# Optimization experiments

Measured on AMD Instinct MI355X. Metric: run time of the kernel, lower is better.

The kernel has to match this reference:

```python
import jax, jax.numpy as jnp
import numpy as np

N, H, W = 2000, 128, 128

def setup_inputs() -> dict:
    key = jax.random.key(0)
    k1, k2, k3, k4 = jax.random.split(key, 4)
    means3D = jax.random.normal(k1, (N, 3), dtype=jnp.float32) * 2.0
    means3D = means3D.at[:, 2].add(10.0)  # put gaussians in front of camera, depth ~in (1,50)
    A = jax.random.normal(k2, (N, 3, 3), dtype=jnp.float32) * 0.1
    covs3d = jnp.einsum('nij,nkj->nik', A, A) + 1e-3 * jnp.eye(3, dtype=jnp.float32)
    colors = jax.random.uniform(k3, (N, 3), dtype=jnp.float32)
    opacities = jax.random.uniform(k4, (N,), dtype=jnp.float32)
    fx = fy = 100.0
    K = jnp.array([[fx, 0.0, W / 2.0], [0.0, fy, H / 2.0], [0.0, 0.0, 1.0]], dtype=jnp.float32)
    R = jnp.eye(3, dtype=jnp.float32)
    t = jnp.zeros((3,), dtype=jnp.float32)
    y, x = jnp.meshgrid(jnp.arange(H, dtype=jnp.float32), jnp.arange(W, dtype=jnp.float32), indexing='ij')
    pixels = jnp.stack([x, y], axis=-1)  # (H, W, 2)
    return {"means3D": means3D, "covs3d": covs3d, "colors": colors,
            "opacities": opacities, "K": K, "R": R, "t": t, "pixels": pixels}

def _render(means3D, covs3d, colors, opacities, K, R, t, pixels):
    # --- projection ---
    cam = means3D @ R.T + t                       # (N,3)
    depths = jnp.clip(cam[:, 2], 1.0, None)       # clamp(min=1.0)
    screen = cam @ K.T
    means2D = screen[:, :2] / screen[:, 2:3]      # (N,2)
    fx, fy = K[0, 0], K[1, 1]
    tx, ty, tz = cam[:, 0], cam[:, 1], cam[:, 2]
    z = jnp.zeros_like(tz)
    J = jnp.stack([jnp.stack([fx / tz, z, -fx * tx / (tz * tz)], -1),
                   jnp.stack([z, fy / tz, -fy * ty / (tz * tz)], -1)], -2)  # (N,2,3)
    covs_cam = jnp.einsum('ij,njk,lk->nil', R, covs3d, R)                   # R C R^T
    covs2D = jnp.einsum('nij,njk,nlk->nil', J, covs_cam, J)                 # (N,2,2)
    valid = (depths > 1.0) & (depths < 50.0)
    # --- depth sort (front to back) ---
    idx = jnp.argsort(depths)
    means2D = means2D[idx]; covs2D = covs2D[idx]
    colors = colors[idx]; opacities = opacities[idx]; valid = valid[idx]
    # --- per-pixel gaussian values ---
    covs2D = covs2D + 1e-4 * jnp.eye(2, dtype=covs2D.dtype)
    a, b = covs2D[:, 0, 0], covs2D[:, 0, 1]
    c, d = covs2D[:, 1, 0], covs2D[:, 1, 1]
    det = a * d - b * c                            # (N,)
    inv = jnp.stack([jnp.stack([d, -b], -1), jnp.stack([-c, a], -1)], -2) / det[:, None, None]
    dx = pixels[None] - means2D[:, None, None, :]  # (N,H,W,2)
    expnum = -jnp.einsum('nhwi,nij,nhwj->nhw', dx, inv, dx)
    gauss = jnp.exp(expnum) / (2.0 * jnp.pi * jnp.sqrt(det))[:, None, None]  # (N,H,W)
    gauss = gauss * valid[:, None, None].astype(gauss.dtype)
    # --- alpha compositing ---
    alphas = opacities[:, None, None] * gauss                   # (N,H,W)
    cum = jnp.cumprod(1.0 - alphas, axis=0)
    trans = jnp.concatenate([jnp.ones((1,) + alphas.shape[1:], alphas.dtype), cum[1:]], axis=0)
    weights = alphas * trans                                    # (N,H,W)
    rendered = jnp.einsum('nhw,nc->hwc', weights, colors)       # (H,W,3)
    return rendered

def reference(means3D, covs3d, colors, opacities, K, R, t, pixels):
    return _render(means3D, covs3d, colors, opacities, K, R, t, pixels)
```

## Files before the change

kernel.cpp:

```cpp
#include <hip/hip_runtime.h>
#include <math.h>

#define NGAUSS 2000
#define IMW 128
#define IMH 128
#define NPIX (IMW*IMH)
#define PSTRIDE 12
#define NW 16
#define SEGSZ ((NGAUSS + NW - 1) / NW)

__device__ inline float rdlane(float x, int l) {
    return __uint_as_float(__builtin_amdgcn_readlane(__float_as_uint(x), l));
}

__global__ __launch_bounds__(64) void preprank_kernel(
    const float* __restrict__ means3D, const float* __restrict__ covs3d,
    const float* __restrict__ colors, const float* __restrict__ opac,
    const float* __restrict__ Km, const float* __restrict__ Rm,
    const float* __restrict__ tv, float* __restrict__ sorted)
{
    int i = blockIdx.x;
    int lane = threadIdx.x;

    float R0 = Rm[0], R1 = Rm[1], R2 = Rm[2];
    float R3 = Rm[3], R4 = Rm[4], R5 = Rm[5];
    float R6 = Rm[6], R7 = Rm[7], R8 = Rm[8];
    float t0 = tv[0], t1v = tv[1], t2 = tv[2];

    float mx = means3D[3*i+0], my = means3D[3*i+1], mz = means3D[3*i+2];
    float di = fmaxf(R6*mx + R7*my + R8*mz + t2, 1.0f);
    int rank = 0;
    for (int j = lane; j < NGAUSS; j += 64) {
        float jx = means3D[3*j+0], jy = means3D[3*j+1], jz = means3D[3*j+2];
        float dj = fmaxf(R6*jx + R7*jy + R8*jz + t2, 1.0f);
        bool lt = (j != i) && ((dj < di) || (dj == di && j < i));
        rank += lt ? 1 : 0;
    }
    #pragma unroll
    for (int o = 32; o > 0; o >>= 1) rank += __shfl_down(rank, o, 64);
    rank = __shfl(rank, 0, 64);

    float camx = R0*mx + R1*my + R2*mz + t0;
    float camy = R3*mx + R4*my + R5*mz + t1v;
    float camz = R6*mx + R7*my + R8*mz + t2;
    float depth = fmaxf(camz, 1.0f);
    bool valid = (depth > 1.0f) && (depth < 50.0f);

    float fx = Km[0], cx = Km[2], fy = Km[4], cy = Km[5];
    float invz = 1.0f / camz;
    float m2x = (fx*camx + cx*camz) * invz;
    float m2y = (fy*camy + cy*camz) * invz;
    float J00 = fx*invz, J02 = -fx*camx*invz*invz;
    float J11 = fy*invz, J12 = -fy*camy*invz*invz;

    float S0 = covs3d[9*i+0], S1 = covs3d[9*i+1], S2 = covs3d[9*i+2];
    float S3 = covs3d[9*i+3], S4 = covs3d[9*i+4], S5 = covs3d[9*i+5];
    float S6 = covs3d[9*i+6], S7 = covs3d[9*i+7], S8 = covs3d[9*i+8];

    float RS0 = R0*S0 + R1*S3 + R2*S6;
    float RS1 = R0*S1 + R1*S4 + R2*S7;
    float RS2 = R0*S2 + R1*S5 + R2*S8;
    float RS3 = R3*S0 + R4*S3 + R5*S6;
    float RS4 = R3*S1 + R4*S4 + R5*S7;
    float RS5 = R3*S2 + R4*S5 + R5*S8;
    float RS6 = R6*S0 + R7*S3 + R8*S6;
    float RS7 = R6*S1 + R7*S4 + R8*S7;
    float RS8 = R6*S2 + R7*S5 + R8*S8;

    float Sc0 = RS0*R0 + RS1*R1 + RS2*R2;
    float Sc1 = RS0*R3 + RS1*R4 + RS2*R5;
    float Sc2 = RS0*R6 + RS1*R7 + RS2*R8;
    float Sc3 = RS3*R0 + RS4*R1 + RS5*R2;
    float Sc4 = RS3*R3 + RS4*R4 + RS5*R5;
    float Sc5 = RS3*R6 + RS4*R7 + RS5*R8;
    float Sc6 = RS6*R0 + RS7*R1 + RS8*R2;
    float Sc7 = RS6*R3 + RS7*R4 + RS8*R5;
    float Sc8 = RS6*R6 + RS7*R7 + RS8*R8;

    float A00 = J00*Sc0 + J02*Sc6;
    float A01 = J00*Sc1 + J02*Sc7;
    float A02 = J00*Sc2 + J02*Sc8;
    float A10 = J11*Sc3 + J12*Sc6;
    float A11 = J11*Sc4 + J12*Sc7;
    float A12 = J11*Sc5 + J12*Sc8;

    float a = A00*J00 + A02*J02 + 1e-4f;
    float b = A01*J11 + A02*J12;
    float c = A10*J00 + A12*J02;
    float d = A11*J11 + A12*J12 + 1e-4f;

    float det = a*d - b*c;
    float invdet = 1.0f / det;
    float q0u = d*invdet;
    float q1u = -(b + c)*invdet;
    float q2u = a*invdet;
    float mh = 0.5f*(q0u + q2u);
    float dh = 0.5f*(q0u - q2u);
    float oh = 0.5f*q1u;
    float lmin = mh - sqrtf(dh*dh + oh*oh);
    const float L2E = 1.4426950408889634f;
    float s_cull = lmin * L2E;
    float q0 = -q0u * L2E;
    float q1 = -q1u * L2E;
    float q2 = -q2u * L2E;
    float c0 = opac[i] * 0.15915494309189535f / sqrtf(det);
    if (!valid) { m2x = 0.f; m2y = 0.f; q0 = 0.f; q1 = 0.f; q2 = 0.f; c0 = 0.f; s_cull = 3.0e38f; }

    float cr = colors[3*i+0], cg = colors[3*i+1], cb = colors[3*i+2];
    if (lane < 3) {
        float4 v = (lane == 0) ? make_float4(m2x, m2y, s_cull, q0)
                 : (lane == 1) ? make_float4(q1, q2, c0, cr)
                               : make_float4(cg, cb, depth, 0.f);
        ((float4*)(sorted + (size_t)rank*PSTRIDE))[lane] = v;
    }
}

__global__ __launch_bounds__(1024) void render_fused(
    const float* __restrict__ sorted, float* __restrict__ out)
{
    extern __shared__ char ldsbuf[];
    float*  mxA  = (float*)ldsbuf;
    float*  myA  = mxA + 2048;
    float*  sA   = myA + 2048;
    float*  q0A  = sA + 2048;
    float4* sp2  = (float4*)(q0A + 2048);
    float4* pOut = sp2 + 2*NGAUSS;

    int tid  = threadIdx.x;
    int lane = tid & 63;
    int w    = tid >> 6;
    int bid  = blockIdx.x;
    int row  = bid >> 1;
    int xoff = (bid & 1) * 64;

    for (int g = tid; g < NGAUSS; g += 1024) {
        const float4* src = (const float4*)(sorted + (size_t)g*PSTRIDE);
        float4 v0 = src[0], v1 = src[1], v2 = src[2];
        mxA[g] = v0.x; myA[g] = v0.y; sA[g] = v0.z; q0A[g] = v0.w;
        sp2[g*2] = v1; sp2[g*2+1] = v2;
    }
    __syncthreads();

    float px = (float)(xoff + lane);
    float py = (float)row;
    float x0 = (float)xoff, x1 = x0 + 63.0f;

    float Cr = 0.f, Cg = 0.f, Cb = 0.f, T = 1.f;

    int segBase = w * SEGSZ;
    int segEnd  = segBase + SEGSZ; if (segEnd > NGAUSS) segEnd = NGAUSS;

    for (int cb = segBase; cb < segEnd; cb += 64) {
        int g = cb + lane;
        float cmx = 0.f, cmy = 0.f, cq0 = 0.f;
        bool keep = false;
        if (g < segEnd) {
            cmx = mxA[g]; cmy = myA[g]; cq0 = q0A[g];
            float cs = sA[g];
            float dxm = fmaxf(0.f, fmaxf(x0 - cmx, cmx - x1));
            float dym = fabsf(py - cmy);
            keep = cs * fmaf(dxm, dxm, dym*dym) <= 24.f;
        }
        float4 v1 = make_float4(0.f,0.f,0.f,0.f), v2 = v1;
        if (keep) { v1 = sp2[g*2]; v2 = sp2[g*2+1]; }
        unsigned long long mask = __ballot(keep);
        while (mask) {
            int b = __builtin_ctzll(mask);
            mask &= mask - 1;
            int gn = cb + b;
            float gmx = rdlane(cmx, b), gmy = rdlane(cmy, b), gq0 = rdlane(cq0, b);
            float gq1 = rdlane(v1.x, b), gq2 = rdlane(v1.y, b), gc0 = rdlane(v1.z, b);
            float gcr = rdlane(v1.w, b), gcg = rdlane(v2.x, b), gcb = rdlane(v2.y, b);
            float dy = py - gmy;
            float u2 = fmaf(gq1, dy, 0.f);
            float dx = px - gmx;
            float e  = fmaf(fmaf(gq0, dx, u2), dx, (gq2*dy)*dy);
            float al = gc0 * exp2f(e);
            float wgt = T * al;
            float sel = (gn == 0) ? 0.f : al;
            float f = fmaf(-sel, wgt, wgt);
            Cr = fmaf(f, gcr, Cr);
            Cg = fmaf(f, gcg, Cg);
            Cb = fmaf(f, gcb, Cb);
            T -= wgt;
        }
    }

    pOut[w*64 + lane] = make_float4(Cr, Cg, Cb, T);
    __syncthreads();

    if (tid < 64) {
        float cR = 0.f, cG = 0.f, cB = 0.f, tA = 1.f;
        #pragma unroll
        for (int s = 0; s < NW; ++s) {
            float4 v = pOut[s*64 + tid];
            cR = fmaf(tA, v.x, cR);
            cG = fmaf(tA, v.y, cG);
            cB = fmaf(tA, v.z, cB);
            tA *= v.w;
        }
        int p = row*IMW + xoff + tid;
        out[3*p+0] = cR; out[3*p+1] = cG; out[3*p+2] = cB;
    }
}

extern "C" void kernel_launch(void* const* d_in, const int* in_sizes, int n_in,
                              void* d_out, int out_size, void* d_ws, size_t ws_size,
                              hipStream_t stream)
{
    const float* means3D = (const float*)d_in[0];
    const float* covs3d  = (const float*)d_in[1];
    const float* colors  = (const float*)d_in[2];
    const float* opac    = (const float*)d_in[3];
    const float* Km      = (const float*)d_in[4];
    const float* Rm      = (const float*)d_in[5];
    const float* tv      = (const float*)d_in[6];

    float* sorted = (float*)d_ws;

    preprank_kernel<<<NGAUSS, 64, 0, stream>>>(
        means3D, covs3d, colors, opac, Km, Rm, tv, sorted);

    size_t ldsBytes = 4*2048*sizeof(float)
                    + (size_t)2*NGAUSS*sizeof(float4)
                    + (size_t)NW*64*sizeof(float4);
    render_fused<<<NPIX/64, 1024, ldsBytes, stream>>>(sorted, (float*)d_out);
}
```

Before: 26.97 us.

## Switch sorted gaussian buffer to SoA and load segments directly into registers

The preprocess kernel now writes ten per-gaussian attributes in structure-of-arrays layout and computes rank with ballot+popcount instead of a shuffle reduction. The render kernel drops the block-wide LDS staging of all 2000 gaussians and the barrier that follows it. Each wave instead loads its 125-gaussian segment straight from global memory into registers as two 64-lane chunks. This removes a large LDS fill per block and shrinks shared memory use, but relies on the hardcoded SEGSZ of at most 128 and repeats global loads across blocks, which should mostly hit cache.

Result: faster. 25.77 us (-4.4%).

```diff
diff --git a/kernel.cpp b/kernel.cpp
--- a/kernel.cpp
+++ b/kernel.cpp
@@ -5,7 +5,6 @@
 #define IMW 128
 #define IMH 128
 #define NPIX (IMW*IMH)
-#define PSTRIDE 12
 #define NW 16
 #define SEGSZ ((NGAUSS + NW - 1) / NW)
 
@@ -17,7 +16,7 @@
     const float* __restrict__ means3D, const float* __restrict__ covs3d,
     const float* __restrict__ colors, const float* __restrict__ opac,
     const float* __restrict__ Km, const float* __restrict__ Rm,
-    const float* __restrict__ tv, float* __restrict__ sorted)
+    const float* __restrict__ tv, float* __restrict__ soa)
 {
     int i = blockIdx.x;
     int lane = threadIdx.x;
@@ -30,15 +29,15 @@
     float mx = means3D[3*i+0], my = means3D[3*i+1], mz = means3D[3*i+2];
     float di = fmaxf(R6*mx + R7*my + R8*mz + t2, 1.0f);
     int rank = 0;
-    for (int j = lane; j < NGAUSS; j += 64) {
-        float jx = means3D[3*j+0], jy = means3D[3*j+1], jz = means3D[3*j+2];
+    for (int base = 0; base < 2048; base += 64) {
+        int j = base + lane;
+        int jc = (j < NGAUSS) ? j : 0;
+        float jx = means3D[3*jc+0], jy = means3D[3*jc+1], jz = means3D[3*jc+2];
         float dj = fmaxf(R6*jx + R7*jy + R8*jz + t2, 1.0f);
-        bool lt = (j != i) && ((dj < di) || (dj == di && j < i));
-        rank += lt ? 1 : 0;
-    }
-    #pragma unroll
-    for (int o = 32; o > 0; o >>= 1) rank += __shfl_down(rank, o, 64);
-    rank = __shfl(rank, 0, 64);
+        bool lt = (j < NGAUSS) && (j != i) &&
+                  ((dj < di) || (dj == di && j < i));
+        rank += (int)__popcll(__ballot(lt));
+    }
 
     float camx = R0*mx + R1*my + R2*mz + t0;
     float camy = R3*mx + R4*my + R5*mz + t1v;
@@ -107,24 +106,23 @@
     if (!valid) { m2x = 0.f; m2y = 0.f; q0 = 0.f; q1 = 0.f; q2 = 0.f; c0 = 0.f; s_cull = 3.0e38f; }
 
     float cr = colors[3*i+0], cg = colors[3*i+1], cb = colors[3*i+2];
-    if (lane < 3) {
-        float4 v = (lane == 0) ? make_float4(m2x, m2y, s_cull, q0)
-                 : (lane == 1) ? make_float4(q1, q2, c0, cr)
-                               : make_float4(cg, cb, depth, 0.f);
-        ((float4*)(sorted + (size_t)rank*PSTRIDE))[lane] = v;
-    }
+    float v = (lane == 0) ? m2x
+            : (lane == 1) ? m2y
+            : (lane == 2) ? s_cull
+            : (lane == 3) ? q0
+            : (lane == 4) ? q1
+            : (lane == 5) ? q2
+            : (lane == 6) ? c0
+            : (lane == 7) ? cr
+            : (lane == 8) ? cg
+                          : cb;
+    if (lane < 10) soa[lane*NGAUSS + rank] = v;
 }
 
 __global__ __launch_bounds__(1024) void render_fused(
-    const float* __restrict__ sorted, float* __restrict__ out)
+    const float* __restrict__ soa, float* __restrict__ out)
 {
-    extern __shared__ char ldsbuf[];
-    float*  mxA  = (float*)ldsbuf;
-    float*  myA  = mxA + 2048;
-    float*  sA   = myA + 2048;
-    float*  q0A  = sA + 2048;
-    float4* sp2  = (float4*)(q0A + 2048);
-    float4* pOut = sp2 + 2*NGAUSS;
+    __shared__ float4 pOut[NW*64];
 
     int tid  = threadIdx.x;
     int lane = tid & 63;
@@ -133,14 +131,6 @@
     int row  = bid >> 1;
     int xoff = (bid & 1) * 64;
 
-    for (int g = tid; g < NGAUSS; g += 1024) {
-        const float4* src = (const float4*)(sorted + (size_t)g*PSTRIDE);
-        float4 v0 = src[0], v1 = src[1], v2 = src[2];
-        mxA[g] = v0.x; myA[g] = v0.y; sA[g] = v0.z; q0A[g] = v0.w;
-        sp2[g*2] = v1; sp2[g*2+1] = v2;
-    }
-    __syncthreads();
-
     float px = (float)(xoff + lane);
     float py = (float)row;
     float x0 = (float)xoff, x1 = x0 + 63.0f;
@@ -148,37 +138,63 @@
     float Cr = 0.f, Cg = 0.f, Cb = 0.f, T = 1.f;
 
     int segBase = w * SEGSZ;
-    int segEnd  = segBase + SEGSZ; if (segEnd > NGAUSS) segEnd = NGAUSS;
-
-    for (int cb = segBase; cb < segEnd; cb += 64) {
-        int g = cb + lane;
-        float cmx = 0.f, cmy = 0.f, cq0 = 0.f;
-        bool keep = false;
-        if (g < segEnd) {
-            cmx = mxA[g]; cmy = myA[g]; cq0 = q0A[g];
-            float cs = sA[g];
-            float dxm = fmaxf(0.f, fmaxf(x0 - cmx, cmx - x1));
-            float dym = fabsf(py - cmy);
-            keep = cs * fmaf(dxm, dxm, dym*dym) <= 24.f;
-        }
-        float4 v1 = make_float4(0.f,0.f,0.f,0.f), v2 = v1;
-        if (keep) { v1 = sp2[g*2]; v2 = sp2[g*2+1]; }
+
+    int gA = segBase + lane;
+    bool vB = (64 + lane) < SEGSZ;
+    int gB = vB ? (segBase + 64 + lane) : segBase;
+    float A0 = soa[0*NGAUSS+gA], A1 = soa[1*NGAUSS+gA], A2 = soa[2*NGAUSS+gA];
+    float A3 = soa[3*NGAUSS+gA], A4 = soa[4*NGAUSS+gA], A5 = soa[5*NGAUSS+gA];
+    float A6 = soa[6*NGAUSS+gA], A7 = soa[7*NGAUSS+gA], A8 = soa[8*NGAUSS+gA];
+    float A9 = soa[9*NGAUSS+gA];
+    float B0 = soa[0*NGAUSS+gB], B1 = soa[1*NGAUSS+gB], B2 = soa[2*NGAUSS+gB];
+    float B3 = soa[3*NGAUSS+gB], B4 = soa[4*NGAUSS+gB], B5 = soa[5*NGAUSS+gB];
+    float B6 = soa[6*NGAUSS+gB], B7 = soa[7*NGAUSS+gB], B8 = soa[8*NGAUSS+gB];
+    float B9 = soa[9*NGAUSS+gB];
+
+    {
+        float dxm = fmaxf(0.f, fmaxf(x0 - A0, A0 - x1));
+        float dym = fabsf(py - A1);
+        bool keep = A2 * fmaf(dxm, dxm, dym*dym) <= 24.f;
         unsigned long long mask = __ballot(keep);
         while (mask) {
             int b = __builtin_ctzll(mask);
             mask &= mask - 1;
-            int gn = cb + b;
-            float gmx = rdlane(cmx, b), gmy = rdlane(cmy, b), gq0 = rdlane(cq0, b);
-            float gq1 = rdlane(v1.x, b), gq2 = rdlane(v1.y, b), gc0 = rdlane(v1.z, b);
-            float gcr = rdlane(v1.w, b), gcg = rdlane(v2.x, b), gcb = rdlane(v2.y, b);
+            int gn = segBase + b;
+            float gmx = rdlane(A0,b), gmy = rdlane(A1,b);
+            float gq0 = rdlane(A3,b), gq1 = rdlane(A4,b), gq2 = rdlane(A5,b);
+            float gc0 = rdlane(A6,b), gcr = rdlane(A7,b);
+            float gcg = rdlane(A8,b), gcb = rdlane(A9,b);
             float dy = py - gmy;
-            float u2 = fmaf(gq1, dy, 0.f);
             float dx = px - gmx;
-            float e  = fmaf(fmaf(gq0, dx, u2), dx, (gq2*dy)*dy);
+            float e  = fmaf(fmaf(gq0, dx, gq1*dy), dx, (gq2*dy)*dy);
             float al = gc0 * exp2f(e);
             float wgt = T * al;
             float sel = (gn == 0) ? 0.f : al;
             float f = fmaf(-sel, wgt, wgt);
+            Cr = fmaf(f, gcr, Cr);
+            Cg = fmaf(f, gcg, Cg);
+            Cb = fmaf(f, gcb, Cb);
+            T -= wgt;
+        }
+    }
+    {
+        float dxm = fmaxf(0.f, fmaxf(x0 - B0, B0 - x1));
+        float dym = fabsf(py - B1);
+        bool keep = vB && (B2 * fmaf(dxm, dxm, dym*dym) <= 24.f);
+        unsigned long long mask = __ballot(keep);
+        while (mask) {
+            int b = __builtin_ctzll(mask);
+            mask &= mask - 1;
+            float gmx = rdlane(B0,b), gmy = rdlane(B1,b);
+            float gq0 = rdlane(B3,b), gq1 = rdlane(B4,b), gq2 = rdlane(B5,b);
+            float gc0 = rdlane(B6,b), gcr = rdlane(B7,b);
+            float gcg = rdlane(B8,b), gcb = rdlane(B9,b);
+            float dy = py - gmy;
+            float dx = px - gmx;
+            float e  = fmaf(fmaf(gq0, dx, gq1*dy), dx, (gq2*dy)*dy);
+            float al = gc0 * exp2f(e);
+            float wgt = T * al;
+            float f = fmaf(-al, wgt, wgt);
             Cr = fmaf(f, gcr, Cr);
             Cg = fmaf(f, gcg, Cg);
             Cb = fmaf(f, gcb, Cb);
@@ -216,13 +232,9 @@
     const float* Rm      = (const float*)d_in[5];
     const float* tv      = (const float*)d_in[6];
 
-    float* sorted = (float*)d_ws;
+    float* soa = (float*)d_ws;
 
     preprank_kernel<<<NGAUSS, 64, 0, stream>>>(
-        means3D, covs3d, colors, opac, Km, Rm, tv, sorted);
-
-    size_t ldsBytes = 4*2048*sizeof(float)
-                    + (size_t)2*NGAUSS*sizeof(float4)
-                    + (size_t)NW*64*sizeof(float4);
-    render_fused<<<NPIX/64, 1024, ldsBytes, stream>>>(sorted, (float*)d_out);
-}
+        means3D, covs3d, colors, opac, Km, Rm, tv, soa);
+    render_fused<<<NPIX/64, 1024, 0, stream>>>(soa, (float*)d_out);
+}
```
